# Optimization experiments

Measured on AMD Instinct MI355X. Metric: run time of the kernel, lower is better.

## Reference

```python
import jax, jax.numpy as jnp
import numpy as np

N_NODES = 8192
D_FEAT = 128
R_BITS = 8      # rows per band
B_BANDS = 64    # number of LSH bands
D_THRESH = 0.25 # cosine-distance threshold from LSH(z, d=0.25, ...)


def setup_inputs() -> dict:
    key = jax.random.key(0)
    k1, k2, k3 = jax.random.split(key, 3)
    z = jax.random.normal(k1, (N_NODES, D_FEAT), dtype=jnp.float32)
    # random hyperplanes for signed-projection LSH: r*b = 512 planes
    H = jax.random.normal(k2, (D_FEAT, R_BITS * B_BANDS), dtype=jnp.float32)
    edge_index = jax.random.randint(k3, (2, N_NODES * 16), 0, N_NODES, dtype=jnp.int64)
    return {"z": z, "H": H, "edge_index": edge_index}


def reference(z, H, edge_index):
    # edge_index is unused by forward_all (kept for signature fidelity).
    N = z.shape[0]
    # --- hyperplane LSH signatures ---
    bits = (z @ H) > 0                              # [N, r*b] bool
    bits = bits.reshape(N, B_BANDS, R_BITS)         # [N, b, r]
    powers = (2 ** jnp.arange(R_BITS)).astype(jnp.int32)
    codes = jnp.sum(bits.astype(jnp.int32) * powers, axis=-1)  # [N, b] band hash codes

    # --- candidate pairs: collide in at least one band (OR over bands) ---
    def band_or(mask, c):  # c: [N] codes for one band
        return mask | (c[:, None] == c[None, :]), None
    collide, _ = jax.lax.scan(band_or, jnp.zeros((N, N), dtype=bool), codes.T)

    # --- exact cosine similarity on candidates ---
    zn = z / jnp.linalg.norm(z, axis=1, keepdims=True)
    S = zn @ zn.T                                   # [N, N] cosine similarity
    dist = 1.0 - S                                  # cosine distance

    eye = jnp.eye(N, dtype=bool)
    # pairs kept by LSH: colliding, within distance threshold, off-diagonal
    keep = collide & (dist < D_THRESH) & (~eye)
    # adjacency[v1, v2] = 1 - dist = cos_sim (sigmoid=True path); identity on diagonal
    A = jnp.where(keep, S, 0.0) + eye.astype(S.dtype)
    return A
```

## Files before the change

### kernel.cpp

```cpp
#include <hip/hip_runtime.h>
#include <hip/hip_bf16.h>

#define N_NODES 8192
#define D_FEAT 128

#define ZN_BYTES (2u * 1024u * 1024u)
#define LIST_CAP 1024
#define NCOMPUTE 442

typedef __bf16 bf16x8 __attribute__((ext_vector_type(8)));
typedef float f32x4 __attribute__((ext_vector_type(4)));

__device__ __forceinline__ void stage_barrier32() {
  asm volatile("s_waitcnt vmcnt(32) lgkmcnt(0)\n\ts_barrier" ::: "memory");
}
__device__ __forceinline__ void vm0_barrier() {
  asm volatile("s_waitcnt vmcnt(0) lgkmcnt(0)\n\ts_barrier" ::: "memory");
}

__device__ __forceinline__ void async_copy16(void* lds, const void* g) {
  __builtin_amdgcn_global_load_lds(
      (const __attribute__((address_space(1))) void*)g,
      (__attribute__((address_space(3))) void*)lds, 16, 0, 0);
}

__device__ __attribute__((noinline)) bool lsh_collide(
    const float* __restrict__ z, const float* __restrict__ H, int i, int j) {
  for (int b = 0; b < 64; ++b) {
    unsigned ci = 0, cj = 0;
    for (int bit = 0; bit < 8; ++bit) {
      int col = b * 8 + bit;
      float di = 0.f, dj = 0.f;
      for (int k = 0; k < D_FEAT; ++k) {
        float h = H[(size_t)k * 512 + col];
        di += z[(size_t)i * D_FEAT + k] * h;
        dj += z[(size_t)j * D_FEAT + k] * h;
      }
      if (di > 0.f) ci |= (1u << bit);
      if (dj > 0.f) cj |= (1u << bit);
    }
    if (ci == cj) return true;
  }
  return false;
}

__device__ __forceinline__ unsigned pack_bf16x2(float x, float y) {
  __hip_bfloat16 bx = __float2bfloat16(x), by = __float2bfloat16(y);
  return (unsigned)(*(unsigned short*)&bx) |
         ((unsigned)(*(unsigned short*)&by) << 16);
}

__global__ __launch_bounds__(256) void norm_kernel(const float* __restrict__ z,
                                                   uint4* __restrict__ zn,
                                                   int* __restrict__ cnt) {
  if (blockIdx.x == 0 && threadIdx.x == 0) *cnt = 0;
  int gt = (int)blockIdx.x * 256 + (int)threadIdx.x;
  int row = gt >> 3, oct = gt & 7;
  const float4* src = (const float4*)(z + (size_t)row * D_FEAT + oct * 16);
  float4 v[4];
#pragma unroll
  for (int c = 0; c < 4; ++c) v[c] = src[c];
  float ss = 0.f;
#pragma unroll
  for (int c = 0; c < 4; ++c)
    ss += v[c].x * v[c].x + v[c].y * v[c].y + v[c].z * v[c].z + v[c].w * v[c].w;
  ss += __shfl_xor(ss, 1);
  ss += __shfl_xor(ss, 2);
  ss += __shfl_xor(ss, 4);
  float inv = rsqrtf(ss);
  int blk = row >> 7, r = row & 127;
  uint4* dst = zn + (size_t)blk * 2048 + r * 16;
#pragma unroll
  for (int c2 = 0; c2 < 2; ++c2) {
    float4 a = v[2 * c2], b = v[2 * c2 + 1];
    uint4 o;
    o.x = pack_bf16x2(a.x * inv, a.y * inv);
    o.y = pack_bf16x2(a.z * inv, a.w * inv);
    o.z = pack_bf16x2(b.x * inv, b.y * inv);
    o.w = pack_bf16x2(b.z * inv, b.w * inv);
    dst[(oct * 2 + c2) ^ (r & 15)] = o;
  }
}

__global__ __launch_bounds__(256, 2) void sim_kernel(const uint4* __restrict__ zn,
                                                     float* __restrict__ out,
                                                     int* __restrict__ cnt,
                                                     int4* __restrict__ list) {
  __shared__ __align__(16) unsigned char smem[65536];

  int tid = threadIdx.x;
  int b = (int)blockIdx.x;

  if (b >= NCOMPUTE) {
    f32x4* outq = (f32x4*)out + ((size_t)b << 15);
#pragma unroll 8
    for (int it = 0; it < 128; ++it) {
      int loc = it * 256 + tid;
      int row = (b << 4) + (loc >> 11);
      int col0 = (loc & 2047) << 2;
      f32x4 v;
      v[0] = (col0 == row) ? 1.0f : 0.0f;
      v[1] = (col0 + 1 == row) ? 1.0f : 0.0f;
      v[2] = (col0 + 2 == row) ? 1.0f : 0.0f;
      v[3] = (col0 + 3 == row) ? 1.0f : 0.0f;
      outq[loc] = v;
    }
    return;
  }

  int a = (int)((sqrtf(40.0f * (float)b + 25.0f) - 5.0f) * 0.1f);
  while (5 * (a + 1) * (a + 2) / 2 <= b) ++a;
  while (a > 0 && 5 * a * (a + 1) / 2 > b) --a;
  int rem = b - 5 * a * (a + 1) / 2;
  int ap1 = a + 1;
  int r = rem / ap1;
  int c = rem - r * ap1;
  int bn = 5 * a + r;
  int bm0 = 5 * c;

  int wv = tid >> 6, lane = tid & 63;
  int wm = (wv >> 1) * 64, wn = (wv & 1) * 64;
  int m16 = lane & 15, g = lane >> 4;

  {
    const uint4* gB = zn + (size_t)bn * 2048;
    const uint4* gA = zn + (size_t)bm0 * 2048;
#pragma unroll
    for (int i = 0; i < 8; ++i) {
      int cc = i * 256 + tid;
      async_copy16(smem + 32768 + cc * 16, gB + cc);
      async_copy16(smem + cc * 16, gA + cc);
    }
  }
  vm0_barrier();

  bf16x8 fbr[16];
  {
    unsigned short (*Bs)[128] = (unsigned short (*)[128])(smem + 32768);
#pragma unroll
    for (int kc = 0; kc < 4; ++kc) {
      int cs = ((kc * 4 + g) ^ m16) * 8;
#pragma unroll
      for (int tt = 0; tt < 4; ++tt)
        fbr[kc * 4 + tt] = *(const bf16x8*)&Bs[wn + tt * 16 + m16][cs];
    }
  }

  for (int t = 0; t < 5; ++t) {
    int bm = bm0 + t;
    bool live = (bm <= bn);
    unsigned char* cur = smem + (t & 1) * 32768;
    unsigned char* nxt = smem + ((t + 1) & 1) * 32768;

    stage_barrier32();

    if (t < 4 && bm + 1 <= bn) {
      const uint4* gA = zn + (size_t)(bm + 1) * 2048;
#pragma unroll
      for (int i = 0; i < 8; ++i) {
        int cc = i * 256 + tid;
        async_copy16(nxt + cc * 16, gA + cc);
      }
    }

    if (t < 4) {
      f32x4* outq = (f32x4*)out + ((size_t)b << 15) + ((size_t)t << 13);
#pragma unroll
      for (int it = 0; it < 32; ++it) {
        int loc = it * 256 + tid;
        int row = (b << 4) + (t << 2) + (loc >> 11);
        int col0 = (loc & 2047) << 2;
        f32x4 v;
        v[0] = (col0 == row) ? 1.0f : 0.0f;
        v[1] = (col0 + 1 == row) ? 1.0f : 0.0f;
        v[2] = (col0 + 2 == row) ? 1.0f : 0.0f;
        v[3] = (col0 + 3 == row) ? 1.0f : 0.0f;
        outq[loc] = v;
      }
    }

    if (live) {
      unsigned short (*As)[128] = (unsigned short (*)[128])cur;
      f32x4 acc[4][4] = {};
#pragma unroll
      for (int kc = 0; kc < 4; ++kc) {
        bf16x8 fa[4];
        int cs = ((kc * 4 + g) ^ m16) * 8;
#pragma unroll
        for (int tt = 0; tt < 4; ++tt)
          fa[tt] = *(const bf16x8*)&As[wm + tt * 16 + m16][cs];
#pragma unroll
        for (int tm = 0; tm < 4; ++tm)
#pragma unroll
          for (int tn = 0; tn < 4; ++tn)
            acc[tm][tn] = __builtin_amdgcn_mfma_f32_16x16x32_bf16(fa[tm], fbr[kc * 4 + tn], acc[tm][tn], 0, 0, 0);
      }

#pragma unroll
      for (int tm = 0; tm < 4; ++tm)
#pragma unroll
        for (int tn = 0; tn < 4; ++tn) {
          f32x4 cc = acc[tm][tn];
          float m4 = fmaxf(fmaxf(cc[0], cc[1]), fmaxf(cc[2], cc[3]));
          if (m4 > 0.75f) {
            int j = bn * 128 + wn + tn * 16 + m16;
#pragma unroll
            for (int rr = 0; rr < 4; ++rr) {
              int i = bm * 128 + wm + tm * 16 + g * 4 + rr;
              if (i != j && cc[rr] > 0.75f) {
                int idx = atomicAdd(cnt, 1);
                if (idx < LIST_CAP)
                  list[idx] = make_int4(i, j, __float_as_int(cc[rr]), 0);
                if (bm < bn) {
                  int idx2 = atomicAdd(cnt, 1);
                  if (idx2 < LIST_CAP)
                    list[idx2] = make_int4(j, i, __float_as_int(cc[rr]), 0);
                }
              }
            }
          }
        }
    }
  }
}

__global__ __launch_bounds__(256) void fixup_kernel(const float* __restrict__ z,
                                                    const float* __restrict__ H,
                                                    const int* __restrict__ cnt,
                                                    const int4* __restrict__ list,
                                                    float* __restrict__ out) {
  int n = *cnt;
  if (n > LIST_CAP) n = LIST_CAP;
  for (int e = (int)threadIdx.x; e < n; e += 256) {
    int i = list[e].x, j = list[e].y;
    float s = __int_as_float(list[e].z);
    if (lsh_collide(z, H, i, j)) out[(size_t)i * N_NODES + j] = s;
  }
}

extern "C" void kernel_launch(void* const* d_in, const int* in_sizes, int n_in,
                              void* d_out, int out_size, void* d_ws, size_t ws_size,
                              hipStream_t stream) {
  const float* z = (const float*)d_in[0];
  const float* H = (const float*)d_in[1];
  float* out = (float*)d_out;
  unsigned char* ws = (unsigned char*)d_ws;
  uint4* zn = (uint4*)ws;
  int* cnt = (int*)(ws + ZN_BYTES);
  int4* list = (int4*)(ws + ZN_BYTES + 16);
  (void)ws_size;

  norm_kernel<<<256, 256, 0, stream>>>(z, zn, cnt);
  sim_kernel<<<512, 256, 0, stream>>>(zn, out, cnt, list);
  fixup_kernel<<<1, 256, 0, stream>>>(z, H, cnt, list, out);
}
```

Measured before the change: 269.1 us.

## Zero output with hipMemsetAsync and write only the diagonal in sim kernel

Removes the interleaved zero/identity stores from the sim kernel and its extra store-only blocks. Instead, a hipMemsetAsync clears the 256 MB output up front, and the diagonal blocks write the ones directly. The grid shrinks to only the compute blocks and the stage barrier waits for all loads. This gives up the overlap between output stores and MFMA compute in exchange for the driver's fill path, which may be close to peak bandwidth.

```diff
diff --git a/kernel.cpp b/kernel.cpp
--- a/kernel.cpp
+++ b/kernel.cpp
@@ -11,9 +11,6 @@
 typedef __bf16 bf16x8 __attribute__((ext_vector_type(8)));
 typedef float f32x4 __attribute__((ext_vector_type(4)));
 
-__device__ __forceinline__ void stage_barrier32() {
-  asm volatile("s_waitcnt vmcnt(32) lgkmcnt(0)\n\ts_barrier" ::: "memory");
-}
 __device__ __forceinline__ void vm0_barrier() {
   asm volatile("s_waitcnt vmcnt(0) lgkmcnt(0)\n\ts_barrier" ::: "memory");
 }
@@ -91,23 +88,6 @@
   int tid = threadIdx.x;
   int b = (int)blockIdx.x;
 
-  if (b >= NCOMPUTE) {
-    f32x4* outq = (f32x4*)out + ((size_t)b << 15);
-#pragma unroll 8
-    for (int it = 0; it < 128; ++it) {
-      int loc = it * 256 + tid;
-      int row = (b << 4) + (loc >> 11);
-      int col0 = (loc & 2047) << 2;
-      f32x4 v;
-      v[0] = (col0 == row) ? 1.0f : 0.0f;
-      v[1] = (col0 + 1 == row) ? 1.0f : 0.0f;
-      v[2] = (col0 + 2 == row) ? 1.0f : 0.0f;
-      v[3] = (col0 + 3 == row) ? 1.0f : 0.0f;
-      outq[loc] = v;
-    }
-    return;
-  }
-
   int a = (int)((sqrtf(40.0f * (float)b + 25.0f) - 5.0f) * 0.1f);
   while (5 * (a + 1) * (a + 2) / 2 <= b) ++a;
   while (a > 0 && 5 * a * (a + 1) / 2 > b) --a;
@@ -152,7 +132,7 @@
     unsigned char* cur = smem + (t & 1) * 32768;
     unsigned char* nxt = smem + ((t + 1) & 1) * 32768;
 
-    stage_barrier32();
+    vm0_barrier();
 
     if (t < 4 && bm + 1 <= bn) {
       const uint4* gA = zn + (size_t)(bm + 1) * 2048;
@@ -163,23 +143,12 @@
       }
     }
 
-    if (t < 4) {
-      f32x4* outq = (f32x4*)out + ((size_t)b << 15) + ((size_t)t << 13);
-#pragma unroll
-      for (int it = 0; it < 32; ++it) {
-        int loc = it * 256 + tid;
-        int row = (b << 4) + (t << 2) + (loc >> 11);
-        int col0 = (loc & 2047) << 2;
-        f32x4 v;
-        v[0] = (col0 == row) ? 1.0f : 0.0f;
-        v[1] = (col0 + 1 == row) ? 1.0f : 0.0f;
-        v[2] = (col0 + 2 == row) ? 1.0f : 0.0f;
-        v[3] = (col0 + 3 == row) ? 1.0f : 0.0f;
-        outq[loc] = v;
-      }
-    }
-
     if (live) {
+      if (bm == bn && tid < 128) {
+        int d = bn * 128 + tid;
+        out[(size_t)d * N_NODES + d] = 1.0f;
+      }
+
       unsigned short (*As)[128] = (unsigned short (*)[128])cur;
       f32x4 acc[4][4] = {};
 #pragma unroll
@@ -250,7 +219,8 @@
   int4* list = (int4*)(ws + ZN_BYTES + 16);
   (void)ws_size;
 
+  hipMemsetAsync(out, 0, (size_t)N_NODES * N_NODES * sizeof(float), stream);
   norm_kernel<<<256, 256, 0, stream>>>(z, zn, cnt);
-  sim_kernel<<<512, 256, 0, stream>>>(zn, out, cnt, list);
+  sim_kernel<<<NCOMPUTE, 256, 0, stream>>>(zn, out, cnt, list);
   fixup_kernel<<<1, 256, 0, stream>>>(z, H, cnt, list, out);
 }
```

New measurement: 273.7 us. No clear change (+1.7%).
